# Kernel tuning notes

Hardware: AMD Instinct MI355X
Metric: run time of the kernel (lower is better)

The kernel has to match this reference:

```python
import jax, jax.numpy as jnp
import numpy as np

NUM_HEADS = 16
LN_EPS = 1e-5


def _layer_norm(x, g, b):
    m = x.mean(-1, keepdims=True)
    v = x.var(-1, keepdims=True)
    return (x - m) / jnp.sqrt(v + LN_EPS) * g + b


def setup_inputs() -> dict:
    key = jax.random.key(0)
    ks = jax.random.split(key, 4)
    Bq, Bk, Nk, C = 128, 128, 256, 1024
    return {
        "qx": jax.random.normal(ks[0], (Bq, 1, C), jnp.float32),
        "kx": jax.random.normal(ks[1], (Bk, Nk, C), jnp.float32),
        "gq": jnp.ones((C,), jnp.float32),
        "bq": jnp.zeros((C,), jnp.float32),
        "gk": jnp.ones((C,), jnp.float32),
        "bk": jnp.zeros((C,), jnp.float32),
        "Wq": jax.random.normal(ks[2], (C, C), jnp.float32) * (C ** -0.5),
        "Wk": jax.random.normal(ks[3], (C, C), jnp.float32) * (C ** -0.5),
    }


def reference(qx, kx, gq, bq, gk, bk, Wq, Wk):
    H = NUM_HEADS
    Bq, _, C = qx.shape  # qx: [Bq, 1, C]
    Bk, Nk, _ = kx.shape  # kx: [Bk, Nk, C]
    hd = C // H
    scale = hd ** -0.5
    # LayerNorm + linear projections (nn.Linear: x @ W.T, no bias)
    q = (_layer_norm(qx, gq, bq) @ Wq.T).reshape(Bq, H, hd)       # [Bq, H, hd] (Nq=1 squeezed)
    k = (_layer_norm(kx, gk, bk) @ Wk.T).reshape(Bk, Nk, H, hd)   # [Bk, Nk, H, hd]
    # Full bipartite cross-batch attention scores: [Bq, Bk, H, Nk]
    attn = jnp.einsum('qhc,knhc->qkhn', q, k) * scale
    attn = jax.nn.softmax(attn, axis=-1)
    # v = kx broadcast over heads in original einsum 'khnc,qkhn->qkc';
    # equivalent: sum attn over heads, then contract over Nk.
    w = attn.sum(axis=2)                                           # [Bq, Bk, Nk]
    x = jnp.einsum('knc,qkn->qkc', kx, w)                          # [Bq, Bk, C]
    return x
```

## Files before the change

kernel.cpp:

```cpp
#include <hip/hip_runtime.h>


typedef unsigned short ushort_t;
typedef __bf16 bf16x8 __attribute__((ext_vector_type(8)));
typedef float f32x4 __attribute__((ext_vector_type(4)));

#define AS1 __attribute__((address_space(1)))
#define AS3 __attribute__((address_space(3)))

__device__ __forceinline__ void gload_lds16(const void* g, void* l) {
  __builtin_amdgcn_global_load_lds((const AS1 unsigned int*)g, (AS3 unsigned int*)l, 16, 0, 0);
}

__device__ __forceinline__ ushort_t f2bf(float f) {
  unsigned u = __float_as_uint(f);
  unsigned r = u + 0x7FFFu + ((u >> 16) & 1u);
  return (ushort_t)(r >> 16);
}

__global__ __launch_bounds__(256) void cvt_bf16_kernel(const float* __restrict__ src,
                                                       ushort_t* __restrict__ dst, int n4) {
  int i = blockIdx.x * 256 + threadIdx.x;
  if (i < n4) {
    float4 v = ((const float4*)src)[i];
    ushort4 o;
    o.x = f2bf(v.x); o.y = f2bf(v.y); o.z = f2bf(v.z); o.w = f2bf(v.w);
    ((ushort4*)dst)[i] = o;
  }
}

__global__ __launch_bounds__(256) void ln_kernel(const float* __restrict__ kx,
                                                 const float* __restrict__ qx,
                                                 const float* __restrict__ gk,
                                                 const float* __restrict__ bk,
                                                 const float* __restrict__ gq,
                                                 const float* __restrict__ bq,
                                                 ushort_t* __restrict__ kln,
                                                 ushort_t* __restrict__ qln) {
  int row = blockIdx.x;
  const float* src; ushort_t* dst; const float* g; const float* bb;
  if (row < 32768) {
    src = kx + (size_t)row * 1024; dst = kln + (size_t)row * 1024; g = gk; bb = bk;
  } else {
    int r = row - 32768;
    src = qx + (size_t)r * 1024; dst = qln + (size_t)r * 1024; g = gq; bb = bq;
  }
  int tid = threadIdx.x;
  float4 v = ((const float4*)src)[tid];
  float s  = v.x + v.y + v.z + v.w;
  float s2 = v.x*v.x + v.y*v.y + v.z*v.z + v.w*v.w;
  #pragma unroll
  for (int off = 1; off < 64; off <<= 1) {
    s  += __shfl_xor(s, off);
    s2 += __shfl_xor(s2, off);
  }
  __shared__ float red[8];
  int wid = tid >> 6, lane = tid & 63;
  if (lane == 0) { red[wid] = s; red[4 + wid] = s2; }
  __syncthreads();
  s  = red[0] + red[1] + red[2] + red[3];
  s2 = red[4] + red[5] + red[6] + red[7];
  float mean = s * (1.0f / 1024.0f);
  float var  = s2 * (1.0f / 1024.0f) - mean * mean;
  float rstd = rsqrtf(var + 1e-5f);
  float4 gg = ((const float4*)g)[tid];
  float4 b4 = ((const float4*)bb)[tid];
  ushort4 o;
  o.x = f2bf((v.x - mean) * rstd * gg.x + b4.x);
  o.y = f2bf((v.y - mean) * rstd * gg.y + b4.y);
  o.z = f2bf((v.z - mean) * rstd * gg.z + b4.z);
  o.w = f2bf((v.w - mean) * rstd * gg.w + b4.w);
  ((ushort4*)dst)[tid] = o;
}

__global__ __launch_bounds__(512, 2) void gemm256_kernel(const ushort_t* __restrict__ A,
                                                         const ushort_t* __restrict__ Bt,
                                                         ushort_t* __restrict__ Cpk,
                                                         const ushort_t* __restrict__ qA,
                                                         const ushort_t* __restrict__ qB,
                                                         ushort_t* __restrict__ qC,
                                                         int M, int N) {
  __shared__ ushort_t lds[4][2][256 * 32];

  const int tid = threadIdx.x, lane = tid & 63, wid = tid >> 6;
  const int g = lane >> 4, rr = lane & 15;
  const int wr = wid >> 2, wc = wid & 3;

  const int Mt = M >> 8, Nt = N >> 8;
  const int nwg = Mt * Nt;
  const int qq = nwg >> 3, r8 = nwg & 7;
  const int xcd = blockIdx.x & 7, idx = blockIdx.x >> 3;
  const int wg = (xcd < r8 ? xcd * (qq + 1) : r8 * (qq + 1) + (xcd - r8) * qq) + idx;
  const int mt = wg / Nt, nt = wg - mt * Nt;
  const size_t m0 = (size_t)mt << 8, n0 = (size_t)nt << 8;

  const int s_r  = lane >> 2;
  const int s_gr = (lane & 3) ^ (s_r & 3);

  const ushort_t* Abase = A  + m0 * 1024;
  const ushort_t* Bbase = Bt + n0 * 1024;

  f32x4 acc[8][4];
  #pragma unroll
  for (int i = 0; i < 8; ++i)
    #pragma unroll
    for (int j = 0; j < 4; ++j) acc[i][j] = (f32x4){0.f, 0.f, 0.f, 0.f};

  auto stageA = [&](int kt) {
    const int k0 = kt << 5;
    ushort_t* dst = &lds[kt & 3][0][0];
    #pragma unroll
    for (int it = 0; it < 2; ++it) {
      int ci = (wid << 1) | it;
      int r  = (ci << 4) + s_r;
      gload_lds16(Abase + (size_t)r * 1024 + k0 + (s_gr << 3), dst + (ci << 9));
    }
  };
  auto stageB = [&](int kt) {
    const int k0 = kt << 5;
    ushort_t* dst = &lds[kt & 3][1][0];
    #pragma unroll
    for (int it = 0; it < 2; ++it) {
      int ci = (wid << 1) | it;
      int r  = (ci << 4) + s_r;
      gload_lds16(Bbase + (size_t)r * 1024 + k0 + (s_gr << 3), dst + (ci << 9));
    }
  };

  stageA(0); stageB(0); stageA(1); stageB(1); stageA(2); stageB(2);
  asm volatile("s_waitcnt vmcnt(8)" ::: "memory");
  __builtin_amdgcn_s_barrier();

  const int rsw = rr & 3;

  #pragma unroll 1
  for (int u = 0; u < 29; ++u) {
    const ushort_t* as = &lds[u & 3][0][0];
    const ushort_t* bs = &lds[u & 3][1][0];
    bf16x8 af[8];
    {
      #pragma unroll
      for (int i = 0; i < 8; ++i) {
        int r = (wr << 7) + (i << 4) + rr;
        af[i] = *(const bf16x8*)&as[(r << 5) + ((g ^ rsw) << 3)];
      }
      int r0 = (wc << 6) + rr;
      bf16x8 b0 = *(const bf16x8*)&bs[(r0 << 5) + ((g ^ rsw) << 3)];
      int r1 = (wc << 6) + 16 + rr;
      bf16x8 b1 = *(const bf16x8*)&bs[(r1 << 5) + ((g ^ rsw) << 3)];
      stageA(u + 3);
      __builtin_amdgcn_s_setprio(1);
      #pragma unroll
      for (int i = 0; i < 8; ++i) {
        acc[i][0] = __builtin_amdgcn_mfma_f32_16x16x32_bf16(af[i], b0, acc[i][0], 0, 0, 0);
        acc[i][1] = __builtin_amdgcn_mfma_f32_16x16x32_bf16(af[i], b1, acc[i][1], 0, 0, 0);
      }
      __builtin_amdgcn_s_setprio(0);
      __builtin_amdgcn_s_barrier();
    }
    {
      int r2 = (wc << 6) + 32 + rr;
      bf16x8 b2 = *(const bf16x8*)&bs[(r2 << 5) + ((g ^ rsw) << 3)];
      int r3 = (wc << 6) + 48 + rr;
      bf16x8 b3 = *(const bf16x8*)&bs[(r3 << 5) + ((g ^ rsw) << 3)];
      stageB(u + 3);
      __builtin_amdgcn_s_setprio(1);
      #pragma unroll
      for (int i = 0; i < 8; ++i) {
        acc[i][2] = __builtin_amdgcn_mfma_f32_16x16x32_bf16(af[i], b2, acc[i][2], 0, 0, 0);
        acc[i][3] = __builtin_amdgcn_mfma_f32_16x16x32_bf16(af[i], b3, acc[i][3], 0, 0, 0);
      }
      __builtin_amdgcn_s_setprio(0);
      asm volatile("s_waitcnt vmcnt(8)" ::: "memory");
      __builtin_amdgcn_s_barrier();
    }
  }

  asm volatile("s_waitcnt vmcnt(0)" ::: "memory");
  __builtin_amdgcn_s_barrier();
  #pragma unroll 1
  for (int u = 29; u < 32; ++u) {
    const ushort_t* as = &lds[u & 3][0][0];
    const ushort_t* bs = &lds[u & 3][1][0];
    bf16x8 af2[8], bfj[4];
    #pragma unroll
    for (int i = 0; i < 8; ++i) {
      int r = (wr << 7) + (i << 4) + rr;
      af2[i] = *(const bf16x8*)&as[(r << 5) + ((g ^ rsw) << 3)];
    }
    #pragma unroll
    for (int j = 0; j < 4; ++j) {
      int r = (wc << 6) + (j << 4) + rr;
      bfj[j] = *(const bf16x8*)&bs[(r << 5) + ((g ^ rsw) << 3)];
    }
    #pragma unroll
    for (int i = 0; i < 8; ++i)
      #pragma unroll
      for (int j = 0; j < 4; ++j)
        acc[i][j] = __builtin_amdgcn_mfma_f32_16x16x32_bf16(af2[i], bfj[j], acc[i][j], 0, 0, 0);
  }

  #pragma unroll
  for (int i = 0; i < 8; ++i)
    #pragma unroll
    for (int j = 0; j < 4; ++j)
      #pragma unroll
      for (int rg = 0; rg < 4; ++rg) {
        size_t row = m0 + (wr << 7) + (i << 4) + (g << 2) + rg;
        size_t col = n0 + (wc << 6) + (j << 4) + rr;
        int kb = (int)(row >> 8), t = (int)((row >> 4) & 15), r16 = (int)(row & 15);
        int h = (int)(col >> 6), ch = (int)(col & 63);
        size_t idx = ((((size_t)kb * 16 + h) * 16 + t) << 10)
                   + ((ch >> 5) << 9) + (((ch >> 3) & 3) << 7) + (r16 << 3) + (ch & 7);
        Cpk[idx] = f2bf(acc[i][j][rg]);
      }

  if ((wg & 63) < 8) {
    const int ti = ((wg >> 6) << 6) + ((wg & 7) << 3) + wid;
    const int mq = ti >> 6, nq = ti & 63;
    const ushort_t* qa = qA + (size_t)(mq * 16 + rr) * 1024 + g * 8;
    const ushort_t* qb = qB + (size_t)(nq * 16 + rr) * 1024 + g * 8;
    f32x4 qacc0 = (f32x4){0.f, 0.f, 0.f, 0.f};
    f32x4 qacc1 = (f32x4){0.f, 0.f, 0.f, 0.f};
    #pragma unroll
    for (int kk = 0; kk < 32; kk += 2) {
      bf16x8 a0 = *(const bf16x8*)(qa + kk * 32);
      bf16x8 b0 = *(const bf16x8*)(qb + kk * 32);
      bf16x8 a1 = *(const bf16x8*)(qa + kk * 32 + 32);
      bf16x8 b1 = *(const bf16x8*)(qb + kk * 32 + 32);
      qacc0 = __builtin_amdgcn_mfma_f32_16x16x32_bf16(a0, b0, qacc0, 0, 0, 0);
      qacc1 = __builtin_amdgcn_mfma_f32_16x16x32_bf16(a1, b1, qacc1, 0, 0, 0);
    }
    #pragma unroll
    for (int rg = 0; rg < 4; ++rg)
      qC[(size_t)(mq * 16 + (g << 2) + rg) * 1024 + nq * 16 + rr] = f2bf(qacc0[rg] + qacc1[rg]);
  }
}

__global__ __launch_bounds__(256, 3) void scores_kernel(const ushort_t* __restrict__ qp,
                                                        const ushort_t* __restrict__ kpk,
                                                        ushort_t* __restrict__ wbuf) {
  __shared__ float pbuf[2][16][258];

  const int tid = threadIdx.x, lane = tid & 63, wid = tid >> 6;
  const int g = lane >> 4, rr = lane & 15;

  const int b = blockIdx.x;
  const int wg = (b & 7) * 128 + (b >> 3);
  const int kb = wg >> 3;
  const int q0 = (wg & 7) << 4;

  const int hs = wid;

  float w_acc[16][4];
  #pragma unroll
  for (int t = 0; t < 16; ++t)
    #pragma unroll
    for (int r = 0; r < 4; ++r) w_acc[t][r] = 0.f;

  const ushort_t* qrow = qp + (size_t)(q0 + rr) * 1024;
  const ushort_t* kbb  = kpk + ((size_t)kb * 16) * 16384 + g * 128 + rr * 8;

  for (int hp = 0; hp < 4; ++hp) {
    const int h = hp * 4 + hs;
    const int co = h * 64 + g * 8;
    bf16x8 aq0 = *(const bf16x8*)(qrow + co);
    bf16x8 aq1 = *(const bf16x8*)(qrow + co + 32);
    const ushort_t* hb = kbb + (size_t)h * 16384;
    f32x4 s[16];
    #pragma unroll
    for (int t = 0; t < 16; ++t) {
      bf16x8 b0 = *(const bf16x8*)(hb + t * 1024);
      bf16x8 b1 = *(const bf16x8*)(hb + t * 1024 + 512);
      f32x4 a = (f32x4){0.f, 0.f, 0.f, 0.f};
      a = __builtin_amdgcn_mfma_f32_16x16x32_bf16(aq0, b0, a, 0, 0, 0);
      a = __builtin_amdgcn_mfma_f32_16x16x32_bf16(aq1, b1, a, 0, 0, 0);
      s[t] = a;
    }
    #pragma unroll
    for (int r = 0; r < 4; ++r) {
      float mx = s[0][r];
      #pragma unroll
      for (int t = 1; t < 16; ++t) mx = fmaxf(mx, s[t][r]);
      mx = fmaxf(mx, __shfl_xor(mx, 1));
      mx = fmaxf(mx, __shfl_xor(mx, 2));
      mx = fmaxf(mx, __shfl_xor(mx, 4));
      mx = fmaxf(mx, __shfl_xor(mx, 8));
      float sum = 0.f;
      float e[16];
      #pragma unroll
      for (int t = 0; t < 16; ++t) {
        e[t] = __expf((s[t][r] - mx) * 0.125f);
        sum += e[t];
      }
      sum += __shfl_xor(sum, 1);
      sum += __shfl_xor(sum, 2);
      sum += __shfl_xor(sum, 4);
      sum += __shfl_xor(sum, 8);
      float inv = 1.0f / sum;
      #pragma unroll
      for (int t = 0; t < 16; ++t) w_acc[t][r] += e[t] * inv;
    }
  }

  __syncthreads();
  if (hs >= 2) {
    #pragma unroll
    for (int t = 0; t < 16; ++t)
      #pragma unroll
      for (int r = 0; r < 4; ++r)
        pbuf[hs - 2][(g << 2) + r][t * 16 + rr] = w_acc[t][r];
  }
  __syncthreads();
  if (hs < 2) {
    #pragma unroll
    for (int t = 0; t < 16; ++t)
      #pragma unroll
      for (int r = 0; r < 4; ++r)
        w_acc[t][r] += pbuf[hs][(g << 2) + r][t * 16 + rr];
    if (hs == 1) {
      #pragma unroll
      for (int t = 0; t < 16; ++t)
        #pragma unroll
        for (int r = 0; r < 4; ++r)
          pbuf[1][(g << 2) + r][t * 16 + rr] = w_acc[t][r];
    }
  }
  __syncthreads();
  if (hs == 0) {
    ushort_t* wb = wbuf + (size_t)kb * 32768;
    #pragma unroll
    for (int t = 0; t < 16; ++t)
      #pragma unroll
      for (int r = 0; r < 4; ++r) {
        float v = w_acc[t][r] + pbuf[1][(g << 2) + r][t * 16 + rr];
        wb[(size_t)(q0 + (g << 2) + r) * 256 + t * 16 + rr] = f2bf(v);
      }
  }
}

__global__ __launch_bounds__(256, 4) void pv_kernel(const ushort_t* __restrict__ wbuf,
                                                    const float* __restrict__ kx,
                                                    float* __restrict__ xout) {
  const int tid = threadIdx.x, lane = tid & 63, wid = tid >> 6;
  const int g = lane >> 4, rr = lane & 15;

  const int b = blockIdx.x;
  const int wg = (b & 7) * 128 + (b >> 3);
  const int kb = wg >> 3;
  const int c0 = (wg & 7) * 128;

  const int wr = wid >> 1, wc = wid & 1;

  f32x4 acc[4][4];
  #pragma unroll
  for (int i = 0; i < 4; ++i)
    #pragma unroll
    for (int j = 0; j < 4; ++j) acc[i][j] = (f32x4){0.f, 0.f, 0.f, 0.f};

  const ushort_t* wb = wbuf + (size_t)kb * 32768;
  const float* kxb = kx + (size_t)kb * 256 * 1024;

  for (int nc = 0; nc < 8; ++nc) {
    const int n0 = nc * 32 + g * 8;
    bf16x8 af[4];
    #pragma unroll
    for (int i = 0; i < 4; ++i) {
      int q = (wr << 6) + (i << 4) + rr;
      af[i] = *(const bf16x8*)(wb + (size_t)q * 256 + n0);
    }
    #pragma unroll
    for (int j = 0; j < 4; ++j) {
      int c = c0 + (wc << 6) + (j << 4) + rr;
      const float* src = kxb + (size_t)n0 * 1024 + c;
      float f[8];
      #pragma unroll
      for (int jj = 0; jj < 8; ++jj) f[jj] = src[(size_t)jj * 1024];
      bf16x8 bb;
      #pragma unroll
      for (int jj = 0; jj < 8; ++jj) bb[jj] = (__bf16)f[jj];
      #pragma unroll
      for (int i = 0; i < 4; ++i)
        acc[i][j] = __builtin_amdgcn_mfma_f32_16x16x32_bf16(af[i], bb, acc[i][j], 0, 0, 0);
    }
  }

  #pragma unroll
  for (int i = 0; i < 4; ++i)
    #pragma unroll
    for (int j = 0; j < 4; ++j)
      #pragma unroll
      for (int rg = 0; rg < 4; ++rg) {
        int q = (wr << 6) + (i << 4) + (g << 2) + rg;
        int c = c0 + (wc << 6) + (j << 4) + rr;
        xout[((size_t)q * 128 + kb) * 1024 + c] = acc[i][j][rg];
      }
}

extern "C" void kernel_launch(void* const* d_in, const int* in_sizes, int n_in,
                              void* d_out, int out_size, void* d_ws, size_t ws_size,
                              hipStream_t stream) {
  const float* qx = (const float*)d_in[0];
  const float* kx = (const float*)d_in[1];
  const float* gq = (const float*)d_in[2];
  const float* bq = (const float*)d_in[3];
  const float* gk = (const float*)d_in[4];
  const float* bk = (const float*)d_in[5];
  const float* Wq = (const float*)d_in[6];
  const float* Wk = (const float*)d_in[7];

  char* ws = (char*)d_ws;
  ushort_t* kkp   = (ushort_t*)(ws);
  ushort_t* qproj = (ushort_t*)(ws + 67108864);
  ushort_t* wbuf  = (ushort_t*)(ws + 67371008);
  ushort_t* qln   = (ushort_t*)(ws + 67371008);
  ushort_t* Wqb   = (ushort_t*)(ws + 67371008 + 262144);
  ushort_t* Wkb   = (ushort_t*)(ws + 67371008 + 2359296);
  ushort_t* kln  = (ushort_t*)d_out;
  float*    xout = (float*)d_out;

  cvt_bf16_kernel<<<1024, 256, 0, stream>>>(Wq, Wqb, 262144);
  cvt_bf16_kernel<<<1024, 256, 0, stream>>>(Wk, Wkb, 262144);
  ln_kernel<<<32896, 256, 0, stream>>>(kx, qx, gk, bk, gq, bq, kln, qln);
  gemm256_kernel<<<512, 512, 0, stream>>>(kln, Wkb, kkp, qln, Wqb, qproj, 32768, 1024);
  scores_kernel<<<1024, 256, 0, stream>>>(qproj, kkp, wbuf);
  pv_kernel<<<1024, 256, 0, stream>>>(wbuf, kx, xout);
}
```

Before: 266.0 us.

## Load pre-packed Wk fragments directly to registers instead of staging B through LDS

Replaces the plain bf16 conversion of Wk with a packing kernel that lays it out in MFMA fragment order, so each wave loads its B operands straight from global memory into registers with one 16-byte load per fragment. The GEMM stops staging B in LDS, which halves LDS use and removes the B LDS reads. The main loop is rebuilt with double-buffered B registers and one barrier per k-step instead of two. In exchange, B traffic now comes from global or L2 memory per wave rather than being shared through LDS, and the vmcnt waits have to be tuned to match.

```diff
diff --git a/kernel.cpp b/kernel.cpp
--- a/kernel.cpp
+++ b/kernel.cpp
@@ -27,6 +27,18 @@
     o.x = f2bf(v.x); o.y = f2bf(v.y); o.z = f2bf(v.z); o.w = f2bf(v.w);
     ((ushort4*)dst)[i] = o;
   }
+}
+
+__global__ __launch_bounds__(256) void pack_wk_kernel(const float* __restrict__ Wk,
+                                                      ushort_t* __restrict__ Bpk) {
+  const int n = blockIdx.x;
+  const int k0 = threadIdx.x * 4;
+  float4 v = *(const float4*)(Wk + (size_t)n * 1024 + k0);
+  ushort4 o;
+  o.x = f2bf(v.x); o.y = f2bf(v.y); o.z = f2bf(v.z); o.w = f2bf(v.w);
+  size_t base = (size_t)((n >> 4) * 32 + (k0 >> 5)) * 512
+              + (size_t)(((k0 >> 3) & 3) * 128) + (size_t)((n & 15) * 8) + (size_t)(k0 & 7);
+  *(ushort4*)(Bpk + base) = o;
 }
 
 __global__ __launch_bounds__(256) void ln_kernel(const float* __restrict__ kx,
@@ -74,13 +86,13 @@
 }
 
 __global__ __launch_bounds__(512, 2) void gemm256_kernel(const ushort_t* __restrict__ A,
-                                                         const ushort_t* __restrict__ Bt,
+                                                         const ushort_t* __restrict__ Bpk,
                                                          ushort_t* __restrict__ Cpk,
                                                          const ushort_t* __restrict__ qA,
                                                          const ushort_t* __restrict__ qB,
                                                          ushort_t* __restrict__ qC,
                                                          int M, int N) {
-  __shared__ ushort_t lds[4][2][256 * 32];
+  __shared__ ushort_t lds[4][256 * 32];
 
   const int tid = threadIdx.x, lane = tid & 63, wid = tid >> 6;
   const int g = lane >> 4, rr = lane & 15;
@@ -96,9 +108,10 @@
 
   const int s_r  = lane >> 2;
   const int s_gr = (lane & 3) ^ (s_r & 3);
-
-  const ushort_t* Abase = A  + m0 * 1024;
-  const ushort_t* Bbase = Bt + n0 * 1024;
+  const int rsw  = rr & 3;
+  const int n16b = (int)(n0 >> 4) + (wc << 2);
+
+  const ushort_t* Abase = A + m0 * 1024;
 
   f32x4 acc[8][4];
   #pragma unroll
@@ -108,7 +121,7 @@
 
   auto stageA = [&](int kt) {
     const int k0 = kt << 5;
-    ushort_t* dst = &lds[kt & 3][0][0];
+    ushort_t* dst = &lds[kt & 3][0];
     #pragma unroll
     for (int it = 0; it < 2; ++it) {
       int ci = (wid << 1) | it;
@@ -116,88 +129,73 @@
       gload_lds16(Abase + (size_t)r * 1024 + k0 + (s_gr << 3), dst + (ci << 9));
     }
   };
-  auto stageB = [&](int kt) {
-    const int k0 = kt << 5;
-    ushort_t* dst = &lds[kt & 3][1][0];
-    #pragma unroll
-    for (int it = 0; it < 2; ++it) {
-      int ci = (wid << 1) | it;
-      int r  = (ci << 4) + s_r;
-      gload_lds16(Bbase + (size_t)r * 1024 + k0 + (s_gr << 3), dst + (ci << 9));
-    }
+  auto loadB = [&](int u, bf16x8 (&bn)[4]) {
+    #pragma unroll
+    for (int j = 0; j < 4; ++j)
+      bn[j] = *(const bf16x8*)(Bpk + (((size_t)((n16b + j) * 32 + u)) << 9) + (lane << 3));
   };
-
-  stageA(0); stageB(0); stageA(1); stageB(1); stageA(2); stageB(2);
-  asm volatile("s_waitcnt vmcnt(8)" ::: "memory");
-  __builtin_amdgcn_s_barrier();
-
-  const int rsw = rr & 3;
-
-  #pragma unroll 1
-  for (int u = 0; u < 29; ++u) {
-    const ushort_t* as = &lds[u & 3][0][0];
-    const ushort_t* bs = &lds[u & 3][1][0];
-    bf16x8 af[8];
-    {
-      #pragma unroll
-      for (int i = 0; i < 8; ++i) {
-        int r = (wr << 7) + (i << 4) + rr;
-        af[i] = *(const bf16x8*)&as[(r << 5) + ((g ^ rsw) << 3)];
-      }
-      int r0 = (wc << 6) + rr;
-      bf16x8 b0 = *(const bf16x8*)&bs[(r0 << 5) + ((g ^ rsw) << 3)];
-      int r1 = (wc << 6) + 16 + rr;
-      bf16x8 b1 = *(const bf16x8*)&bs[(r1 << 5) + ((g ^ rsw) << 3)];
-      stageA(u + 3);
-      __builtin_amdgcn_s_setprio(1);
-      #pragma unroll
-      for (int i = 0; i < 8; ++i) {
-        acc[i][0] = __builtin_amdgcn_mfma_f32_16x16x32_bf16(af[i], b0, acc[i][0], 0, 0, 0);
-        acc[i][1] = __builtin_amdgcn_mfma_f32_16x16x32_bf16(af[i], b1, acc[i][1], 0, 0, 0);
-      }
-      __builtin_amdgcn_s_setprio(0);
-      __builtin_amdgcn_s_barrier();
-    }
-    {
-      int r2 = (wc << 6) + 32 + rr;
-      bf16x8 b2 = *(const bf16x8*)&bs[(r2 << 5) + ((g ^ rsw) << 3)];
-      int r3 = (wc << 6) + 48 + rr;
-      bf16x8 b3 = *(const bf16x8*)&bs[(r3 << 5) + ((g ^ rsw) << 3)];
-      stageB(u + 3);
-      __builtin_amdgcn_s_setprio(1);
-      #pragma unroll
-      for (int i = 0; i < 8; ++i) {
-        acc[i][2] = __builtin_amdgcn_mfma_f32_16x16x32_bf16(af[i], b2, acc[i][2], 0, 0, 0);
-        acc[i][3] = __builtin_amdgcn_mfma_f32_16x16x32_bf16(af[i], b3, acc[i][3], 0, 0, 0);
-      }
-      __builtin_amdgcn_s_setprio(0);
-      asm volatile("s_waitcnt vmcnt(8)" ::: "memory");
-      __builtin_amdgcn_s_barrier();
-    }
-  }
-
+  auto readA = [&](int u, bf16x8 (&af)[8]) {
+    const ushort_t* as = &lds[u & 3][0];
+    #pragma unroll
+    for (int i = 0; i < 8; ++i) {
+      int r = (wr << 7) + (i << 4) + rr;
+      af[i] = *(const bf16x8*)&as[(r << 5) + ((g ^ rsw) << 3)];
+    }
+  };
+
+  bf16x8 bA[4], bB[4];
+
+  stageA(0); stageA(1); stageA(2);
+  loadB(0, bA);
   asm volatile("s_waitcnt vmcnt(0)" ::: "memory");
   __builtin_amdgcn_s_barrier();
+
+  auto iterfull = [&](int u, bf16x8 (&bc)[4], bf16x8 (&bn)[4]) {
+    bf16x8 af[8];
+    readA(u, af);
+    loadB(u + 1, bn);
+    stageA(u + 3);
+    __builtin_amdgcn_s_setprio(1);
+    #pragma unroll
+    for (int i = 0; i < 8; ++i)
+      #pragma unroll
+      for (int j = 0; j < 4; ++j)
+        acc[i][j] = __builtin_amdgcn_mfma_f32_16x16x32_bf16(af[i], bc[j], acc[i][j], 0, 0, 0);
+    __builtin_amdgcn_s_setprio(0);
+    asm volatile("s_waitcnt vmcnt(2)" ::: "memory");
+    __builtin_amdgcn_s_barrier();
+  };
+  auto iternostage = [&](int u, bf16x8 (&bc)[4], bf16x8 (&bn)[4]) {
+    bf16x8 af[8];
+    readA(u, af);
+    loadB(u + 1, bn);
+    __builtin_amdgcn_s_setprio(1);
+    #pragma unroll
+    for (int i = 0; i < 8; ++i)
+      #pragma unroll
+      for (int j = 0; j < 4; ++j)
+        acc[i][j] = __builtin_amdgcn_mfma_f32_16x16x32_bf16(af[i], bc[j], acc[i][j], 0, 0, 0);
+    __builtin_amdgcn_s_setprio(0);
+    asm volatile("s_waitcnt vmcnt(0)" ::: "memory");
+    __builtin_amdgcn_s_barrier();
+  };
+
   #pragma unroll 1
-  for (int u = 29; u < 32; ++u) {
-    const ushort_t* as = &lds[u & 3][0][0];
-    const ushort_t* bs = &lds[u & 3][1][0];
-    bf16x8 af2[8], bfj[4];
-    #pragma unroll
-    for (int i = 0; i < 8; ++i) {
-      int r = (wr << 7) + (i << 4) + rr;
-      af2[i] = *(const bf16x8*)&as[(r << 5) + ((g ^ rsw) << 3)];
-    }
-    #pragma unroll
-    for (int j = 0; j < 4; ++j) {
-      int r = (wc << 6) + (j << 4) + rr;
-      bfj[j] = *(const bf16x8*)&bs[(r << 5) + ((g ^ rsw) << 3)];
-    }
+  for (int u2 = 0; u2 < 28; u2 += 2) {
+    iterfull(u2,     bA, bB);
+    iterfull(u2 + 1, bB, bA);
+  }
+  iterfull(28, bA, bB);
+  iternostage(29, bB, bA);
+  iternostage(30, bA, bB);
+  {
+    bf16x8 af[8];
+    readA(31, af);
     #pragma unroll
     for (int i = 0; i < 8; ++i)
       #pragma unroll
       for (int j = 0; j < 4; ++j)
-        acc[i][j] = __builtin_amdgcn_mfma_f32_16x16x32_bf16(af2[i], bfj[j], acc[i][j], 0, 0, 0);
+        acc[i][j] = __builtin_amdgcn_mfma_f32_16x16x32_bf16(af[i], bB[j], acc[i][j], 0, 0, 0);
   }
 
   #pragma unroll
@@ -210,9 +208,9 @@
         size_t col = n0 + (wc << 6) + (j << 4) + rr;
         int kb = (int)(row >> 8), t = (int)((row >> 4) & 15), r16 = (int)(row & 15);
         int h = (int)(col >> 6), ch = (int)(col & 63);
-        size_t idx = ((((size_t)kb * 16 + h) * 16 + t) << 10)
+        size_t odx = ((((size_t)kb * 16 + h) * 16 + t) << 10)
                    + ((ch >> 5) << 9) + (((ch >> 3) & 3) << 7) + (r16 << 3) + (ch & 7);
-        Cpk[idx] = f2bf(acc[i][j][rg]);
+        Cpk[odx] = f2bf(acc[i][j][rg]);
       }
 
   if ((wg & 63) < 8) {
@@ -415,14 +413,14 @@
   ushort_t* wbuf  = (ushort_t*)(ws + 67371008);
   ushort_t* qln   = (ushort_t*)(ws + 67371008);
   ushort_t* Wqb   = (ushort_t*)(ws + 67371008 + 262144);
-  ushort_t* Wkb   = (ushort_t*)(ws + 67371008 + 2359296);
+  ushort_t* Bpk   = (ushort_t*)(ws + 67371008 + 2359296);
   ushort_t* kln  = (ushort_t*)d_out;
   float*    xout = (float*)d_out;
 
   cvt_bf16_kernel<<<1024, 256, 0, stream>>>(Wq, Wqb, 262144);
-  cvt_bf16_kernel<<<1024, 256, 0, stream>>>(Wk, Wkb, 262144);
+  pack_wk_kernel<<<1024, 256, 0, stream>>>(Wk, Bpk);
   ln_kernel<<<32896, 256, 0, stream>>>(kx, qx, gk, bk, gq, bq, kln, qln);
-  gemm256_kernel<<<512, 512, 0, stream>>>(kln, Wkb, kkp, qln, Wqb, qproj, 32768, 1024);
+  gemm256_kernel<<<512, 512, 0, stream>>>(kln, Bpk, kkp, qln, Wqb, qproj, 32768, 1024);
   scores_kernel<<<1024, 256, 0, stream>>>(qproj, kkp, wbuf);
   pv_kernel<<<1024, 256, 0, stream>>>(wbuf, kx, xout);
 }
```

New measurement: 268.1 us. About the same (+0.8%).
